# Kernel tuning notes

Measured on AMD Instinct MI355X. Metric: run time of the kernel, lower is better.

Reference implementation:

```python
import jax, jax.numpy as jnp
import numpy as np

NVIEW = 6
N = 6400        # nodes (hardcoded in source: torch.empty(6400, 6))
D = 2048        # input_dim
H = 512         # hidden_dim
C = 256         # common_dim
E = 204800      # edges per view (avg degree 32)


def spmm(h, src, dst, val):
    # sparse_adj @ h : gather source rows, scale by edge value, scatter-add to dst
    msg = val[:, None] * h[src]              # [E, F]
    return jax.ops.segment_sum(msg, dst, num_segments=N)


def setup_inputs() -> dict:
    key = jax.random.key(0)
    ks = jax.random.split(key, 12)
    x = jax.random.normal(ks[0], (NVIEW, N, D), dtype=jnp.float32)
    adj_src = jax.random.randint(ks[1], (NVIEW, E), 0, N, dtype=jnp.int32)
    adj_dst = jax.random.randint(ks[2], (NVIEW, E), 0, N, dtype=jnp.int32)
    # normalized-adjacency-like positive values, scaled ~1/degree to keep activations sane
    adj_val = jax.random.uniform(ks[3], (NVIEW, E), dtype=jnp.float32) / 32.0
    # glorot-ish scaling
    Wb = jax.random.normal(ks[4], (NVIEW, D, H), dtype=jnp.float32) / np.sqrt(D)
    Wo = jax.random.normal(ks[5], (NVIEW, H, H), dtype=jnp.float32) / np.sqrt(H)
    Wf = jax.random.normal(ks[6], (NVIEW, H, H), dtype=jnp.float32) / np.sqrt(H)
    Wc0 = jax.random.normal(ks[7], (D, C), dtype=jnp.float32) / np.sqrt(D)
    Wc1 = jax.random.normal(ks[8], (C, C), dtype=jnp.float32) / np.sqrt(C)
    Wc2 = jax.random.normal(ks[9], (C, C), dtype=jnp.float32) / np.sqrt(C)
    gate_w = jax.random.normal(ks[10], (NVIEW, NVIEW, H + C), dtype=jnp.float32) / np.sqrt(H + C)
    gate_b = jax.random.normal(ks[11], (NVIEW, NVIEW), dtype=jnp.float32) * 0.01
    return {"x": x, "adj_val": adj_val, "Wb": Wb, "Wo": Wo, "Wf": Wf,
            "Wc0": Wc0, "Wc1": Wc1, "Wc2": Wc2, "gate_w": gate_w, "gate_b": gate_b,
            "adj_src": adj_src, "adj_dst": adj_dst}


def reference(x, adj_val, Wb, Wo, Wf, Wc0, Wc1, Wc2, gate_w, gate_b, adj_src, adj_dst):
    zs = []
    for v in range(NVIEW):
        src, dst, val = adj_src[v], adj_dst[v], adj_val[v]
        # view-specific 3-layer GCN (relu, relu, identity)
        hidden = jax.nn.relu(spmm(x[v] @ Wb[v], src, dst, val))   # [N, H]
        mid    = jax.nn.relu(spmm(hidden @ Wo[v], src, dst, val)) # [N, H]
        final  = spmm(mid @ Wf[v], src, dst, val)                 # [N, H]
        z_v = (hidden + mid + final) / 3.0                        # layer_agg == 'mean'
        # shared common 3-layer GCN
        c = jax.nn.relu(spmm(x[v] @ Wc0, src, dst, val))          # [N, C]
        c = jax.nn.relu(spmm(c @ Wc1, src, dst, val))
        c = jax.nn.relu(spmm(c @ Wc2, src, dst, val))
        zs.append(jnp.concatenate([c, z_v], axis=1))              # [N, C+H]
    Z = jnp.stack(zs, axis=0)                                     # [V, N, C+H]
    # gate scores: score_k[:, i] = Linear_{k,i}(z_i)
    scores = jnp.einsum('inf,kif->kni', Z, gate_w) + gate_b[:, None, :]  # [V, N, V]
    scores = jax.nn.softmax(scores, axis=-1)
    z_global = jnp.einsum('kni,inf->knf', scores, Z)              # [V, N, C+H]
    return (z_global, Z)
```

## Files before the change

### kernel.cpp

```cpp
#include <hip/hip_runtime.h>
#include <hip/hip_bf16.h>

#define NVIEW 6
#define NN    6400
#define DD    2048
#define HH    512
#define CC    256
#define EE    204800
#define ZF    768

typedef __bf16 bf16x8 __attribute__((ext_vector_type(8)));
typedef __bf16 bf16x4 __attribute__((ext_vector_type(4)));
typedef float  f32x4  __attribute__((ext_vector_type(4)));

__device__ __forceinline__ float b2f(unsigned short u) {
  union { unsigned int i; float f; } c; c.i = ((unsigned int)u) << 16; return c.f;
}

__device__ __forceinline__ void glds16(const void* g, void* l) {
  __builtin_amdgcn_global_load_lds((const __attribute__((address_space(1))) void*)g,
                                   (__attribute__((address_space(3))) void*)l, 16, 0, 0);
}

__global__ void k_hist(const int* __restrict__ dst, int* __restrict__ hist) {
  int e = blockIdx.x * 256 + threadIdx.x;
  int v = blockIdx.y;
  if (e < EE) atomicAdd(&hist[v * NN + dst[(size_t)v * EE + e]], 1);
}

__global__ __launch_bounds__(1024) void k_scan(const int* __restrict__ hist,
                                               int* __restrict__ rp) {
  int v = blockIdx.x;
  const int* h = hist + v * NN;
  int* r = rp + v * (NN + 1);
  __shared__ int part[1024];
  int t = threadIdx.x;
  const int CH = 7;
  int base = t * CH;
  int loc[CH];
  int s = 0;
#pragma unroll
  for (int i = 0; i < CH; i++) {
    int idx = base + i;
    int val = (idx < NN) ? h[idx] : 0;
    loc[i] = s;
    s += val;
  }
  part[t] = s;
  __syncthreads();
  for (int off = 1; off < 1024; off <<= 1) {
    int x = (t >= off) ? part[t - off] : 0;
    __syncthreads();
    part[t] += x;
    __syncthreads();
  }
  int pre = (t == 0) ? 0 : part[t - 1];
#pragma unroll
  for (int i = 0; i < CH; i++) {
    int idx = base + i;
    if (idx < NN) r[idx] = pre + loc[i];
  }
  if (t == 1023) r[NN] = part[1023];
}

__global__ void k_cursor(const int* __restrict__ rp, int* __restrict__ cur) {
  int i = blockIdx.x * 256 + threadIdx.x;
  if (i < NVIEW * NN) {
    int v = i / NN, n = i - v * NN;
    cur[i] = rp[v * (NN + 1) + n];
  }
}

__global__ void k_scatter(const int* __restrict__ src, const int* __restrict__ dstA,
                          const float* __restrict__ val, int* __restrict__ cur,
                          int2* __restrict__ sedge) {
  int e = blockIdx.x * 256 + threadIdx.x;
  int v = blockIdx.y;
  if (e < EE) {
    size_t idx = (size_t)v * EE + e;
    int d = dstA[idx];
    int pos = atomicAdd(&cur[v * NN + d], 1);
    sedge[(size_t)v * EE + pos] = make_int2(src[idx], __float_as_int(val[idx]));
  }
}

__global__ __launch_bounds__(256) void k_cvt(const float* __restrict__ in,
                                             __bf16* __restrict__ out) {
  size_t i = (size_t)blockIdx.x * 256 + threadIdx.x;
  float4 q = ((const float4*)in)[i];
  bf16x4 o;
  o[0] = (__bf16)q.x; o[1] = (__bf16)q.y; o[2] = (__bf16)q.z; o[3] = (__bf16)q.w;
  *(bf16x4*)(out + i * 4) = o;
}

__global__ __launch_bounds__(256) void k_tw(const float* __restrict__ in,
                                            __bf16* __restrict__ out, int K, int N,
                                            size_t inSB, size_t outSB) {
  __shared__ float sh[32][33];
  int b = blockIdx.z;
  int k0 = blockIdx.x * 32, n0 = blockIdx.y * 32;
  int tx = threadIdx.x & 31, ty = threadIdx.x >> 5;
  const float* I = in + (size_t)b * inSB;
  __bf16* O = out + (size_t)b * outSB;
#pragma unroll
  for (int r = 0; r < 4; r++)
    sh[ty + r * 8][tx] = I[(size_t)(k0 + ty + r * 8) * N + n0 + tx];
  __syncthreads();
#pragma unroll
  for (int r = 0; r < 4; r++)
    O[(size_t)(n0 + ty + r * 8) * K + k0 + tx] = (__bf16)sh[tx][ty + r * 8];
}

__global__ __launch_bounds__(512, 2) void k_g256(
    const __bf16* __restrict__ A, const __bf16* __restrict__ BT,
    __bf16* __restrict__ C, int K, int Nc, int nbn, int bpv, int wPerView)
{
  __shared__ __bf16 ldsv[65536];
  int tid = threadIdx.x, lane = tid & 63, w = tid >> 6;

  int nwg = gridDim.x;
  int q8 = nwg >> 3, r8 = nwg & 7;
  int orig = blockIdx.x;
  int xcd = orig & 7, j = orig >> 3;
  int swz = (xcd < r8 ? xcd * (q8 + 1) : r8 * (q8 + 1) + (xcd - r8) * q8) + j;
  int v = swz / bpv; int rr = swz - v * bpv;
  int bm = rr / nbn; int bn = rr - bm * nbn;

  const __bf16* Av = A + (size_t)v * NN * K + (size_t)(bm * 256) * K;
  const __bf16* Bv = BT + (wPerView ? (size_t)v * Nc * K : 0) + (size_t)(bn * 256) * K;

  f32x4 acc[8][4];
#pragma unroll
  for (int m = 0; m < 8; m++)
#pragma unroll
    for (int n = 0; n < 4; n++) acc[m][n] = (f32x4){0.f, 0.f, 0.f, 0.f};

  const int wr = (w >> 2) * 128, wc = (w & 3) * 64;
  const int gq = lane >> 4, l15 = lane & 15;

#define STAGE_UNIT(Gp, LOFF, KH, KT)                                          \
  {                                                                           \
    _Pragma("unroll")                                                         \
    for (int g2 = 0; g2 < 2; g2++) {                                          \
      int u = g2 * 512 + tid;                                                 \
      int row_ = ((u >> 5) << 3) | (u & 7);                                   \
      int kkgl_ = (u >> 3) & 3;                                               \
      glds16(Gp + (size_t)row_ * K + (KT) * 64 + (KH) * 32 + kkgl_ * 8,       \
             ldsv + (LOFF) + (KH) * 8192 + u * 8);                            \
    }                                                                         \
  }

#define PH_READS(KK, MH, LOADB)                                               \
  {                                                                           \
    _Pragma("unroll")                                                         \
    for (int m = 0; m < 4; m++) {                                             \
      int ra = wr + (MH) * 64 + m * 16 + l15;                                 \
      aF[m] = *(const bf16x8*)&Ab[(KK) * 8192 + (ra >> 3) * 256 + gq * 64 +   \
                                  (ra & 7) * 8];                              \
    }                                                                         \
    if (LOADB) {                                                              \
      _Pragma("unroll")                                                       \
      for (int n = 0; n < 4; n++) {                                           \
        int rb = wc + n * 16 + l15;                                           \
        bF[n] = *(const bf16x8*)&Bb[(KK) * 8192 + (rb >> 3) * 256 + gq * 64 + \
                                    (rb & 7) * 8];                            \
      }                                                                       \
    }                                                                         \
  }

#define PH_MFMA(MH)                                                           \
  {                                                                           \
    __builtin_amdgcn_s_barrier();                                             \
    asm volatile("s_waitcnt lgkmcnt(0)" ::: "memory");                        \
    __builtin_amdgcn_sched_barrier(0);                                        \
    __builtin_amdgcn_s_setprio(1);                                            \
    _Pragma("unroll")                                                         \
    for (int m = 0; m < 4; m++)                                               \
      _Pragma("unroll")                                                       \
      for (int n = 0; n < 4; n++)                                             \
        acc[(MH) * 4 + m][n] = __builtin_amdgcn_mfma_f32_16x16x32_bf16(       \
            aF[m], bF[n], acc[(MH) * 4 + m][n], 0, 0, 0);                     \
    __builtin_amdgcn_s_setprio(0);                                            \
    __builtin_amdgcn_s_barrier();                                             \
  }

  const int nt = K >> 6;
  const int ni = nt >> 1;

  STAGE_UNIT(Av, 0,     0, 0);
  STAGE_UNIT(Bv, 16384, 0, 0);
  STAGE_UNIT(Av, 0,     1, 0);
  STAGE_UNIT(Bv, 16384, 1, 0);
  STAGE_UNIT(Av, 32768, 0, 1);
  STAGE_UNIT(Bv, 49152, 0, 1);
  asm volatile("s_waitcnt vmcnt(4)" ::: "memory");
  __builtin_amdgcn_s_barrier();

  bf16x8 aF[4], bF[4];
  for (int i = 0; i < ni; ++i) {
    int t1 = 2 * i + 1, t2 = 2 * i + 2, t3 = 2 * i + 3;
    bool more = (i + 1 < ni);
    const __bf16* Ab = ldsv;
    const __bf16* Bb = ldsv + 16384;
    PH_READS(0, 0, true);
    STAGE_UNIT(Av, 32768, 1, t1);
    asm volatile("s_waitcnt vmcnt(6)" ::: "memory");
    PH_MFMA(0);
    PH_READS(0, 1, false); STAGE_UNIT(Bv, 49152, 1, t1);              PH_MFMA(1);
    PH_READS(1, 0, true);
    if (more) {
      STAGE_UNIT(Av, 0, 0, t2);
      asm volatile("s_waitcnt vmcnt(6)" ::: "memory");
    } else {
      asm volatile("s_waitcnt vmcnt(4)" ::: "memory");
    }
    PH_MFMA(0);
    PH_READS(1, 1, false); if (more) STAGE_UNIT(Bv, 16384, 0, t2);    PH_MFMA(1);
    Ab = ldsv + 32768; Bb = ldsv + 49152;
    PH_READS(0, 0, true);
    if (more) {
      STAGE_UNIT(Av, 0, 1, t2);
      asm volatile("s_waitcnt vmcnt(6)" ::: "memory");
    } else {
      asm volatile("s_waitcnt vmcnt(0)" ::: "memory");
    }
    PH_MFMA(0);
    PH_READS(0, 1, false); if (more) STAGE_UNIT(Bv, 16384, 1, t2);    PH_MFMA(1);
    PH_READS(1, 0, true);
    if (more) {
      STAGE_UNIT(Av, 32768, 0, t3);
      asm volatile("s_waitcnt vmcnt(6)" ::: "memory");
    }
    PH_MFMA(0);
    PH_READS(1, 1, false);
    if (more) STAGE_UNIT(Bv, 49152, 0, t3);
    PH_MFMA(1);
  }

#undef STAGE_UNIT
#undef PH_READS
#undef PH_MFMA

  __bf16* Cv = C + (size_t)v * NN * Nc;
#pragma unroll
  for (int m = 0; m < 8; m++) {
    int rbase = bm * 256 + wr + m * 16 + (lane >> 4) * 4;
#pragma unroll
    for (int q = 0; q < 4; q++) {
      __bf16* cp = Cv + (size_t)(rbase + q) * Nc + bn * 256 + wc + l15;
#pragma unroll
      for (int n = 0; n < 4; n++) cp[n * 16] = (__bf16)acc[m][n][q];
    }
  }
}

template <int LDIN, int FOFF, int F, int CHUNKS, int MODE>
__global__ __launch_bounds__(256) void k_spmm(
    const __bf16* __restrict__ in, const int* __restrict__ rp,
    const int2* __restrict__ sedge, void* __restrict__ out,
    const __bf16* __restrict__ h1, const __bf16* __restrict__ h2)
{
  int id = blockIdx.x;
  int s = id & 7, j = id >> 3;
  int ch, v, rowblk;
  if (CHUNKS == 2) {
    ch = s >> 2; int q = s & 3;
    v = j / 400; int t = j - v * 400;
    rowblk = t * 4 + q;
  } else {
    ch = 0;
    v = j / 200; int t = j - v * 200;
    rowblk = t * 8 + s;
  }
  int wid = threadIdx.x >> 6, lane = threadIdx.x & 63;
  int n = rowblk * 4 + wid;
  int f0 = ch * 256 + lane * 4;

  const int* rpv = rp + v * (NN + 1);
  int e = rpv[n], end = rpv[n + 1];
  const int2* ev = sedge + (size_t)v * EE;
  const __bf16* inv = in + (size_t)v * NN * LDIN + FOFF;

  float a0 = 0.f, a1 = 0.f, a2 = 0.f, a3 = 0.f;
  for (; e + 8 <= end; e += 8) {
    int2 ee[8]; ushort4 rrv[8];
#pragma unroll
    for (int u = 0; u < 8; u++) ee[u] = ev[e + u];
#pragma unroll
    for (int u = 0; u < 8; u++)
      rrv[u] = *(const ushort4*)(inv + (size_t)ee[u].x * LDIN + f0);
#pragma unroll
    for (int u = 0; u < 8; u++) {
      float wv = __int_as_float(ee[u].y);
      a0 += wv * b2f(rrv[u].x); a1 += wv * b2f(rrv[u].y);
      a2 += wv * b2f(rrv[u].z); a3 += wv * b2f(rrv[u].w);
    }
  }
  if (e + 4 <= end) {
    int2 ee[4]; ushort4 rrv[4];
#pragma unroll
    for (int u = 0; u < 4; u++) ee[u] = ev[e + u];
#pragma unroll
    for (int u = 0; u < 4; u++)
      rrv[u] = *(const ushort4*)(inv + (size_t)ee[u].x * LDIN + f0);
#pragma unroll
    for (int u = 0; u < 4; u++) {
      float wv = __int_as_float(ee[u].y);
      a0 += wv * b2f(rrv[u].x); a1 += wv * b2f(rrv[u].y);
      a2 += wv * b2f(rrv[u].z); a3 += wv * b2f(rrv[u].w);
    }
    e += 4;
  }
  for (; e < end; ++e) {
    int2 e0 = ev[e];
    float w0 = __int_as_float(e0.y);
    ushort4 r0 = *(const ushort4*)(inv + (size_t)e0.x * LDIN + f0);
    a0 += w0 * b2f(r0.x); a1 += w0 * b2f(r0.y);
    a2 += w0 * b2f(r0.z); a3 += w0 * b2f(r0.w);
  }

  if (MODE == 0) {
    __bf16* o = (__bf16*)out + ((size_t)v * NN + n) * F + f0;
    bf16x4 ov;
    ov[0] = (__bf16)fmaxf(a0, 0.f); ov[1] = (__bf16)fmaxf(a1, 0.f);
    ov[2] = (__bf16)fmaxf(a2, 0.f); ov[3] = (__bf16)fmaxf(a3, 0.f);
    *(bf16x4*)o = ov;
  } else if (MODE == 1) {
    float* o = (float*)out + ((size_t)v * NN + n) * ZF + f0;
    o[0] = fmaxf(a0, 0.f); o[1] = fmaxf(a1, 0.f);
    o[2] = fmaxf(a2, 0.f); o[3] = fmaxf(a3, 0.f);
  } else {
    const __bf16* hh = h1 + ((size_t)v * NN + n) * 512 + f0;
    const __bf16* mm = h2 + ((size_t)v * NN + n) * 512 + f0;
    ushort4 hu = *(const ushort4*)hh;
    ushort4 mu = *(const ushort4*)mm;
    float* o = (float*)out + ((size_t)v * NN + n) * ZF + CC + f0;
    o[0] = (b2f(hu.x) + b2f(mu.x) + a0) * (1.f / 3.f);
    o[1] = (b2f(hu.y) + b2f(mu.y) + a1) * (1.f / 3.f);
    o[2] = (b2f(hu.z) + b2f(mu.z) + a2) * (1.f / 3.f);
    o[3] = (b2f(hu.w) + b2f(mu.w) + a3) * (1.f / 3.f);
  }
}

__global__ __launch_bounds__(256) void k_gate(
    const float* __restrict__ Z, const float* __restrict__ gw,
    const float* __restrict__ gb, float* __restrict__ zg)
{
  __shared__ float Zl[NVIEW * ZF];
  __shared__ float sred[36];
  __shared__ float pl[36];
  int n = blockIdx.x, tid = threadIdx.x;

  for (int idx = tid; idx < NVIEW * ZF; idx += 256) {
    int i = idx / ZF, f = idx - i * ZF;
    Zl[idx] = Z[((size_t)i * NN + n) * ZF + f];
  }
  if (tid < 36) sred[tid] = 0.f;
  __syncthreads();

  float acc[36];
#pragma unroll
  for (int p = 0; p < 36; p++) acc[p] = 0.f;
#pragma unroll
  for (int q = 0; q < 3; q++) {
    int f = tid + q * 256;
    float zv[NVIEW];
#pragma unroll
    for (int i = 0; i < NVIEW; i++) zv[i] = Zl[i * ZF + f];
#pragma unroll
    for (int k = 0; k < NVIEW; k++)
#pragma unroll
      for (int i = 0; i < NVIEW; i++)
        acc[k * 6 + i] += zv[i] * gw[(k * 6 + i) * ZF + f];
  }
  int lane = tid & 63;
#pragma unroll
  for (int p = 0; p < 36; p++) {
    float x = acc[p];
    x += __shfl_down(x, 32, 64);
    x += __shfl_down(x, 16, 64);
    x += __shfl_down(x, 8, 64);
    x += __shfl_down(x, 4, 64);
    x += __shfl_down(x, 2, 64);
    x += __shfl_down(x, 1, 64);
    if (lane == 0) atomicAdd(&sred[p], x);
  }
  __syncthreads();

  if (tid < NVIEW) {
    int k = tid;
    float sc[NVIEW];
    float mx = -1e30f;
#pragma unroll
    for (int i = 0; i < NVIEW; i++) {
      sc[i] = sred[k * 6 + i] + gb[k * 6 + i];
      mx = fmaxf(mx, sc[i]);
    }
    float sum = 0.f;
#pragma unroll
    for (int i = 0; i < NVIEW; i++) { sc[i] = __expf(sc[i] - mx); sum += sc[i]; }
    float inv = 1.f / sum;
#pragma unroll
    for (int i = 0; i < NVIEW; i++) pl[k * 6 + i] = sc[i] * inv;
  }
  __syncthreads();

#pragma unroll
  for (int q = 0; q < 3; q++) {
    int f = tid + q * 256;
    float zv[NVIEW];
#pragma unroll
    for (int i = 0; i < NVIEW; i++) zv[i] = Zl[i * ZF + f];
#pragma unroll
    for (int k = 0; k < NVIEW; k++) {
      float o = 0.f;
#pragma unroll
      for (int i = 0; i < NVIEW; i++) o += pl[k * 6 + i] * zv[i];
      zg[((size_t)k * NN + n) * ZF + f] = o;
    }
  }
}

extern "C" void kernel_launch(void* const* d_in, const int* in_sizes, int n_in,
                              void* d_out, int out_size, void* d_ws, size_t ws_size,
                              hipStream_t stream) {
  const float* x    = (const float*)d_in[0];
  const float* aval = (const float*)d_in[1];
  const float* Wb   = (const float*)d_in[2];
  const float* Wo   = (const float*)d_in[3];
  const float* Wf   = (const float*)d_in[4];
  const float* Wc0  = (const float*)d_in[5];
  const float* Wc1  = (const float*)d_in[6];
  const float* Wc2  = (const float*)d_in[7];
  const float* gw   = (const float*)d_in[8];
  const float* gb   = (const float*)d_in[9];
  const int*   asrc = (const int*)d_in[10];
  const int*   adst = (const int*)d_in[11];

  float* zg = (float*)d_out;
  float* Z  = zg + (size_t)NVIEW * NN * ZF;
  __bf16* xb = (__bf16*)d_out;

  char* w = (char*)d_ws;
  auto alloc = [&](size_t bytes) {
    char* p = w;
    w += (bytes + 255) & ~(size_t)255;
    return p;
  };
  int*    hist  = (int*)alloc((size_t)NVIEW * NN * 4);
  int*    rp    = (int*)alloc((size_t)NVIEW * (NN + 1) * 4);
  int2*   sedge = (int2*)alloc((size_t)NVIEW * EE * 8);
  __bf16* Wfu   = (__bf16*)alloc((size_t)NVIEW * ZF * DD * 2);
  __bf16* WoT   = (__bf16*)alloc((size_t)NVIEW * HH * HH * 2);
  __bf16* WfT   = (__bf16*)alloc((size_t)NVIEW * HH * HH * 2);
  __bf16* Wc1T  = (__bf16*)alloc((size_t)CC * CC * 2);
  __bf16* Wc2T  = (__bf16*)alloc((size_t)CC * CC * 2);
  __bf16* tf768 = (__bf16*)alloc((size_t)NVIEW * NN * ZF * 2);
  __bf16* t512b = (__bf16*)alloc((size_t)NVIEW * NN * HH * 2);
  __bf16* hidb  = (__bf16*)alloc((size_t)NVIEW * NN * HH * 2);
  __bf16* midb  = (__bf16*)alloc((size_t)NVIEW * NN * HH * 2);
  __bf16* tcb   = (__bf16*)alloc((size_t)NVIEW * NN * CC * 2);
  __bf16* cbb   = (__bf16*)alloc((size_t)NVIEW * NN * CC * 2);

  (void)hipMemsetAsync(hist, 0, (size_t)NVIEW * NN * 4, stream);
  k_hist<<<dim3(800, NVIEW), 256, 0, stream>>>(adst, hist);
  k_scan<<<NVIEW, 1024, 0, stream>>>(hist, rp);
  k_cursor<<<150, 256, 0, stream>>>(rp, hist);
  k_scatter<<<dim3(800, NVIEW), 256, 0, stream>>>(asrc, adst, aval, hist, sedge);

  k_cvt<<<76800, 256, 0, stream>>>(x, xb);
  k_tw<<<dim3(64, 16, NVIEW), 256, 0, stream>>>(Wb, Wfu, DD, HH,
                                                (size_t)DD * HH, (size_t)ZF * DD);
  k_tw<<<dim3(64, 8, NVIEW), 256, 0, stream>>>(Wc0, Wfu + (size_t)HH * DD, DD, CC,
                                               0, (size_t)ZF * DD);
  k_tw<<<dim3(16, 16, NVIEW), 256, 0, stream>>>(Wo, WoT, HH, HH,
                                                (size_t)HH * HH, (size_t)HH * HH);
  k_tw<<<dim3(16, 16, NVIEW), 256, 0, stream>>>(Wf, WfT, HH, HH,
                                                (size_t)HH * HH, (size_t)HH * HH);
  k_tw<<<dim3(8, 8, 1), 256, 0, stream>>>(Wc1, Wc1T, CC, CC, 0, 0);
  k_tw<<<dim3(8, 8, 1), 256, 0, stream>>>(Wc2, Wc2T, CC, CC, 0, 0);

  k_g256<<<450, 512, 0, stream>>>(xb, Wfu, tf768, DD, ZF, 3, 75, 1);
  k_spmm<768, 0, 512, 2, 0><<<19200, 256, 0, stream>>>(tf768, rp, sedge, hidb, nullptr, nullptr);
  k_spmm<768, 512, 256, 1, 0><<<9600, 256, 0, stream>>>(tf768, rp, sedge, cbb, nullptr, nullptr);

  k_g256<<<300, 512, 0, stream>>>(hidb, WoT, t512b, HH, HH, 2, 50, 1);
  k_spmm<512, 0, 512, 2, 0><<<19200, 256, 0, stream>>>(t512b, rp, sedge, midb, nullptr, nullptr);
  k_g256<<<150, 512, 0, stream>>>(cbb, Wc1T, tcb, CC, CC, 1, 25, 0);
  k_spmm<256, 0, 256, 1, 0><<<9600, 256, 0, stream>>>(tcb, rp, sedge, cbb, nullptr, nullptr);
  k_g256<<<300, 512, 0, stream>>>(midb, WfT, t512b, HH, HH, 2, 50, 1);
  k_spmm<512, 0, 512, 2, 2><<<19200, 256, 0, stream>>>(t512b, rp, sedge, Z, hidb, midb);
  k_g256<<<150, 512, 0, stream>>>(cbb, Wc2T, tcb, CC, CC, 1, 25, 0);
  k_spmm<256, 0, 256, 1, 1><<<9600, 256, 0, stream>>>(tcb, rp, sedge, Z, nullptr, nullptr);

  k_gate<<<NN, 256, 0, stream>>>(Z, gw, gb, zg);
}
```

Baseline: 1.165 ms.

## Merge independent kernels into combined launches to cut launch count

Folds the histogram, x conversion and all weight transposes into one prep kernel, and writes the scan output straight into the cursor array so the separate cursor kernel goes away. The independent view-specific and common GEMMs and SpMMs are paired into single launches that dispatch on block index. This removes many small launches and their serialization gaps, and lets the smaller common-branch work fill the GPU alongside the larger branch. The cost is branchy combined kernels whose register and LDS use is set by the larger path, and the in-place cbb SpMM now runs in the same launch as other work.

```diff
diff --git a/kernel.cpp b/kernel.cpp
--- a/kernel.cpp
+++ b/kernel.cpp
@@ -22,14 +22,73 @@
                                    (__attribute__((address_space(3))) void*)l, 16, 0, 0);
 }
 
-__global__ void k_hist(const int* __restrict__ dst, int* __restrict__ hist) {
-  int e = blockIdx.x * 256 + threadIdx.x;
-  int v = blockIdx.y;
-  if (e < EE) atomicAdd(&hist[v * NN + dst[(size_t)v * EE + e]], 1);
+__global__ __launch_bounds__(256) void k_prep(
+    const int* __restrict__ dst, int* __restrict__ hist,
+    const float* __restrict__ x, __bf16* __restrict__ xb,
+    const float* __restrict__ Wb, const float* __restrict__ Wc0,
+    __bf16* __restrict__ Wfu,
+    const float* __restrict__ Wo, const float* __restrict__ Wf,
+    __bf16* __restrict__ WoT, __bf16* __restrict__ WfT,
+    const float* __restrict__ Wc1, const float* __restrict__ Wc2,
+    __bf16* __restrict__ Wc1T, __bf16* __restrict__ Wc2T)
+{
+  __shared__ float sh[32][33];
+  int id = blockIdx.x;
+  if (id < 4800) {
+    int e = (id % 800) * 256 + threadIdx.x;
+    int v = id / 800;
+    if (e < EE) atomicAdd(&hist[v * NN + dst[(size_t)v * EE + e]], 1);
+    return;
+  }
+  id -= 4800;
+  if (id < 76800) {
+    size_t i = (size_t)id * 256 + threadIdx.x;
+    float4 q = ((const float4*)x)[i];
+    bf16x4 o;
+    o[0] = (__bf16)q.x; o[1] = (__bf16)q.y; o[2] = (__bf16)q.z; o[3] = (__bf16)q.w;
+    *(bf16x4*)(xb + i * 4) = o;
+    return;
+  }
+  id -= 76800;
+  const float* I; __bf16* O; int K, N, bx, by;
+  if (id < 6144) {
+    bx = id & 63; int r = id >> 6; by = r & 15; int b = r >> 4;
+    I = Wb + (size_t)b * DD * HH;
+    O = Wfu + (size_t)b * ZF * DD;
+    K = DD; N = HH;
+  } else if (id < 6144 + 3072) {
+    id -= 6144;
+    bx = id & 63; int r = id >> 6; by = r & 7; int b = r >> 3;
+    I = Wc0;
+    O = Wfu + (size_t)HH * DD + (size_t)b * ZF * DD;
+    K = DD; N = CC;
+  } else if (id < 6144 + 3072 + 3072) {
+    id -= 6144 + 3072;
+    bx = id & 15; int r = id >> 4; by = r & 15; int z = r >> 4;
+    if (z < 6) { I = Wo + (size_t)z * HH * HH; O = WoT + (size_t)z * HH * HH; }
+    else       { I = Wf + (size_t)(z - 6) * HH * HH; O = WfT + (size_t)(z - 6) * HH * HH; }
+    K = HH; N = HH;
+  } else {
+    id -= 6144 + 3072 + 3072;
+    bx = id & 7; int r = id >> 3; by = r & 7; int z = r >> 3;
+    I = (z == 0) ? Wc1 : Wc2;
+    O = (z == 0) ? Wc1T : Wc2T;
+    K = CC; N = CC;
+  }
+  int k0 = bx * 32, n0 = by * 32;
+  int tx = threadIdx.x & 31, ty = threadIdx.x >> 5;
+#pragma unroll
+  for (int r = 0; r < 4; r++)
+    sh[ty + r * 8][tx] = I[(size_t)(k0 + ty + r * 8) * N + n0 + tx];
+  __syncthreads();
+#pragma unroll
+  for (int r = 0; r < 4; r++)
+    O[(size_t)(n0 + ty + r * 8) * K + k0 + tx] = (__bf16)sh[tx][ty + r * 8];
 }
 
 __global__ __launch_bounds__(1024) void k_scan(const int* __restrict__ hist,
-                                               int* __restrict__ rp) {
+                                               int* __restrict__ rp,
+                                               int* __restrict__ cur) {
   int v = blockIdx.x;
   const int* h = hist + v * NN;
   int* r = rp + v * (NN + 1);
@@ -58,17 +117,13 @@
 #pragma unroll
   for (int i = 0; i < CH; i++) {
     int idx = base + i;
-    if (idx < NN) r[idx] = pre + loc[i];
+    if (idx < NN) {
+      int val = pre + loc[i];
+      r[idx] = val;
+      cur[v * NN + idx] = val;
+    }
   }
   if (t == 1023) r[NN] = part[1023];
-}
-
-__global__ void k_cursor(const int* __restrict__ rp, int* __restrict__ cur) {
-  int i = blockIdx.x * 256 + threadIdx.x;
-  if (i < NVIEW * NN) {
-    int v = i / NN, n = i - v * NN;
-    cur[i] = rp[v * (NN + 1) + n];
-  }
 }
 
 __global__ void k_scatter(const int* __restrict__ src, const int* __restrict__ dstA,
@@ -84,43 +139,14 @@
   }
 }
 
-__global__ __launch_bounds__(256) void k_cvt(const float* __restrict__ in,
-                                             __bf16* __restrict__ out) {
-  size_t i = (size_t)blockIdx.x * 256 + threadIdx.x;
-  float4 q = ((const float4*)in)[i];
-  bf16x4 o;
-  o[0] = (__bf16)q.x; o[1] = (__bf16)q.y; o[2] = (__bf16)q.z; o[3] = (__bf16)q.w;
-  *(bf16x4*)(out + i * 4) = o;
-}
-
-__global__ __launch_bounds__(256) void k_tw(const float* __restrict__ in,
-                                            __bf16* __restrict__ out, int K, int N,
-                                            size_t inSB, size_t outSB) {
-  __shared__ float sh[32][33];
-  int b = blockIdx.z;
-  int k0 = blockIdx.x * 32, n0 = blockIdx.y * 32;
-  int tx = threadIdx.x & 31, ty = threadIdx.x >> 5;
-  const float* I = in + (size_t)b * inSB;
-  __bf16* O = out + (size_t)b * outSB;
-#pragma unroll
-  for (int r = 0; r < 4; r++)
-    sh[ty + r * 8][tx] = I[(size_t)(k0 + ty + r * 8) * N + n0 + tx];
-  __syncthreads();
-#pragma unroll
-  for (int r = 0; r < 4; r++)
-    O[(size_t)(n0 + ty + r * 8) * K + k0 + tx] = (__bf16)sh[tx][ty + r * 8];
-}
-
-__global__ __launch_bounds__(512, 2) void k_g256(
+__device__ __forceinline__ void g256_body(
     const __bf16* __restrict__ A, const __bf16* __restrict__ BT,
-    __bf16* __restrict__ C, int K, int Nc, int nbn, int bpv, int wPerView)
-{
-  __shared__ __bf16 ldsv[65536];
+    __bf16* __restrict__ C, int K, int Nc, int nbn, int bpv, int wPerView,
+    int orig, int nwg, __bf16* ldsv)
+{
   int tid = threadIdx.x, lane = tid & 63, w = tid >> 6;
 
-  int nwg = gridDim.x;
   int q8 = nwg >> 3, r8 = nwg & 7;
-  int orig = blockIdx.x;
   int xcd = orig & 7, j = orig >> 3;
   int swz = (xcd < r8 ? xcd * (q8 + 1) : r8 * (q8 + 1) + (xcd - r8) * q8) + j;
   int v = swz / bpv; int rr = swz - v * bpv;
@@ -254,13 +280,34 @@
   }
 }
 
+__global__ __launch_bounds__(512, 2) void k_g256s(
+    const __bf16* __restrict__ A, const __bf16* __restrict__ BT,
+    __bf16* __restrict__ C, int K, int Nc, int nbn, int bpv, int wPerView)
+{
+  __shared__ __bf16 ldsv[65536];
+  g256_body(A, BT, C, K, Nc, nbn, bpv, wPerView, blockIdx.x, gridDim.x, ldsv);
+}
+
+__global__ __launch_bounds__(512, 2) void k_g256p(
+    const __bf16* A1, const __bf16* B1, __bf16* C1,
+    int K1, int Nc1, int nbn1, int bpv1, int w1, int S1,
+    const __bf16* A2, const __bf16* B2, __bf16* C2,
+    int K2, int Nc2, int nbn2, int bpv2, int w2)
+{
+  __shared__ __bf16 ldsv[65536];
+  if ((int)blockIdx.x < S1)
+    g256_body(A1, B1, C1, K1, Nc1, nbn1, bpv1, w1, blockIdx.x, S1, ldsv);
+  else
+    g256_body(A2, B2, C2, K2, Nc2, nbn2, bpv2, w2, blockIdx.x - S1,
+              gridDim.x - S1, ldsv);
+}
+
 template <int LDIN, int FOFF, int F, int CHUNKS, int MODE>
-__global__ __launch_bounds__(256) void k_spmm(
-    const __bf16* __restrict__ in, const int* __restrict__ rp,
+__device__ __forceinline__ void spmm_body(
+    int id, const __bf16* __restrict__ in, const int* __restrict__ rp,
     const int2* __restrict__ sedge, void* __restrict__ out,
     const __bf16* __restrict__ h1, const __bf16* __restrict__ h2)
 {
-  int id = blockIdx.x;
   int s = id & 7, j = id >> 3;
   int ch, v, rowblk;
   if (CHUNKS == 2) {
@@ -342,6 +389,20 @@
   }
 }
 
+template <int S1,
+          int LD1, int FO1, int F1, int CH1, int MO1,
+          int LD2, int FO2, int F2, int CH2, int MO2>
+__global__ __launch_bounds__(256) void k_spmm2(
+    const __bf16* __restrict__ in1, void* __restrict__ out1,
+    const __bf16* __restrict__ in2, void* __restrict__ out2,
+    const int* __restrict__ rp, const int2* __restrict__ sedge,
+    const __bf16* __restrict__ h1, const __bf16* __restrict__ h2)
+{
+  int id = blockIdx.x;
+  if (id < S1) spmm_body<LD1, FO1, F1, CH1, MO1>(id, in1, rp, sedge, out1, h1, h2);
+  else         spmm_body<LD2, FO2, F2, CH2, MO2>(id - S1, in2, rp, sedge, out2, h1, h2);
+}
+
 __global__ __launch_bounds__(256) void k_gate(
     const float* __restrict__ Z, const float* __restrict__ gw,
     const float* __restrict__ gb, float* __restrict__ zg)
@@ -463,35 +524,23 @@
   __bf16* cbb   = (__bf16*)alloc((size_t)NVIEW * NN * CC * 2);
 
   (void)hipMemsetAsync(hist, 0, (size_t)NVIEW * NN * 4, stream);
-  k_hist<<<dim3(800, NVIEW), 256, 0, stream>>>(adst, hist);
-  k_scan<<<NVIEW, 1024, 0, stream>>>(hist, rp);
-  k_cursor<<<150, 256, 0, stream>>>(rp, hist);
+  k_prep<<<94016, 256, 0, stream>>>(adst, hist, x, xb, Wb, Wc0, Wfu,
+                                    Wo, Wf, WoT, WfT, Wc1, Wc2, Wc1T, Wc2T);
+  k_scan<<<NVIEW, 1024, 0, stream>>>(hist, rp, hist);
   k_scatter<<<dim3(800, NVIEW), 256, 0, stream>>>(asrc, adst, aval, hist, sedge);
 
-  k_cvt<<<76800, 256, 0, stream>>>(x, xb);
-  k_tw<<<dim3(64, 16, NVIEW), 256, 0, stream>>>(Wb, Wfu, DD, HH,
-                                                (size_t)DD * HH, (size_t)ZF * DD);
-  k_tw<<<dim3(64, 8, NVIEW), 256, 0, stream>>>(Wc0, Wfu + (size_t)HH * DD, DD, CC,
-                                               0, (size_t)ZF * DD);
-  k_tw<<<dim3(16, 16, NVIEW), 256, 0, stream>>>(Wo, WoT, HH, HH,
-                                                (size_t)HH * HH, (size_t)HH * HH);
-  k_tw<<<dim3(16, 16, NVIEW), 256, 0, stream>>>(Wf, WfT, HH, HH,
-                                                (size_t)HH * HH, (size_t)HH * HH);
-  k_tw<<<dim3(8, 8, 1), 256, 0, stream>>>(Wc1, Wc1T, CC, CC, 0, 0);
-  k_tw<<<dim3(8, 8, 1), 256, 0, stream>>>(Wc2, Wc2T, CC, CC, 0, 0);
-
-  k_g256<<<450, 512, 0, stream>>>(xb, Wfu, tf768, DD, ZF, 3, 75, 1);
-  k_spmm<768, 0, 512, 2, 0><<<19200, 256, 0, stream>>>(tf768, rp, sedge, hidb, nullptr, nullptr);
-  k_spmm<768, 512, 256, 1, 0><<<9600, 256, 0, stream>>>(tf768, rp, sedge, cbb, nullptr, nullptr);
-
-  k_g256<<<300, 512, 0, stream>>>(hidb, WoT, t512b, HH, HH, 2, 50, 1);
-  k_spmm<512, 0, 512, 2, 0><<<19200, 256, 0, stream>>>(t512b, rp, sedge, midb, nullptr, nullptr);
-  k_g256<<<150, 512, 0, stream>>>(cbb, Wc1T, tcb, CC, CC, 1, 25, 0);
-  k_spmm<256, 0, 256, 1, 0><<<9600, 256, 0, stream>>>(tcb, rp, sedge, cbb, nullptr, nullptr);
-  k_g256<<<300, 512, 0, stream>>>(midb, WfT, t512b, HH, HH, 2, 50, 1);
-  k_spmm<512, 0, 512, 2, 2><<<19200, 256, 0, stream>>>(t512b, rp, sedge, Z, hidb, midb);
-  k_g256<<<150, 512, 0, stream>>>(cbb, Wc2T, tcb, CC, CC, 1, 25, 0);
-  k_spmm<256, 0, 256, 1, 1><<<9600, 256, 0, stream>>>(tcb, rp, sedge, Z, nullptr, nullptr);
+  k_g256s<<<450, 512, 0, stream>>>(xb, Wfu, tf768, DD, ZF, 3, 75, 1);
+
+  k_spmm2<19200, 768, 0, 512, 2, 0, 768, 512, 256, 1, 0>
+      <<<28800, 256, 0, stream>>>(tf768, hidb, tf768, cbb, rp, sedge, nullptr, nullptr);
+  k_g256p<<<450, 512, 0, stream>>>(hidb, WoT, t512b, HH, HH, 2, 50, 1, 300,
+                                   cbb, Wc1T, tcb, CC, CC, 1, 25, 0);
+  k_spmm2<19200, 512, 0, 512, 2, 0, 256, 0, 256, 1, 0>
+      <<<28800, 256, 0, stream>>>(t512b, midb, tcb, cbb, rp, sedge, nullptr, nullptr);
+  k_g256p<<<450, 512, 0, stream>>>(midb, WfT, t512b, HH, HH, 2, 50, 1, 300,
+                                   cbb, Wc2T, tcb, CC, CC, 1, 25, 0);
+  k_spmm2<19200, 512, 0, 512, 2, 2, 256, 0, 256, 1, 1>
+      <<<28800, 256, 0, stream>>>(t512b, Z, tcb, Z, rp, sedge, hidb, midb);
 
   k_gate<<<NN, 256, 0, stream>>>(Z, gw, gb, zg);
 }
```

Result: faster. 1.100 ms (-5.6%).
